# Optimization experiments

Measured on AMD Instinct MI355X. Metric: run time of the kernel, lower is better.

The kernel has to match this reference:

```python
import jax, jax.numpy as jnp
import numpy as np

WS = 8      # window size
SS = 4      # shift size
NH = 4      # num heads
EPS = 1e-5
MLP_RATIO = 4


def _win_part(x, ws):
    # x: [B,D,H,W,C] -> [B*nD*nH*nW, ws^3, C]
    B, D, H, W, C = x.shape
    x = x.reshape(B, D // ws, ws, H // ws, ws, W // ws, ws, C)
    x = x.transpose(0, 1, 3, 5, 2, 4, 6, 7)
    return x.reshape(-1, ws * ws * ws, C)


def _win_rev(w, ws, B, D, H, W):
    C = w.shape[-1]
    x = w.reshape(B, D // ws, H // ws, W // ws, ws, ws, ws, C)
    x = x.transpose(0, 1, 4, 2, 5, 3, 6, 7)
    return x.reshape(B, D, H, W, C)


def _ln(x, g, b):
    m = jnp.mean(x, axis=-1, keepdims=True)
    v = jnp.mean((x - m) ** 2, axis=-1, keepdims=True)
    return (x - m) / jnp.sqrt(v + EPS) * g + b


def _rel_index(ws):
    coords = np.stack(np.meshgrid(np.arange(ws), np.arange(ws), np.arange(ws), indexing='ij'))  # [3,ws,ws,ws]
    cf = coords.reshape(3, -1)                      # [3, ws^3]
    rel = (cf[:, :, None] - cf[:, None, :]).transpose(1, 2, 0) + (ws - 1)  # [N,N,3]
    return rel[..., 0] * (2 * ws - 1) ** 2 + rel[..., 1] * (2 * ws - 1) + rel[..., 2]


def _attn_mask(D, H, W, ws, ss):
    img = np.zeros((1, D, H, W, 1), dtype=np.float32)
    cnt = 0
    sl = (slice(0, -ws), slice(-ws, -ss), slice(-ss, None))
    for d in sl:
        for h in sl:
            for w in sl:
                img[:, d, h, w, :] = cnt
                cnt += 1
    mw = np.asarray(_win_part(jnp.asarray(img), ws))[..., 0]  # [nW, ws^3]
    diff = mw[:, None, :] - mw[:, :, None]
    return np.where(diff != 0, -100.0, 0.0).astype(np.float32)


def setup_inputs() -> dict:
    key = jax.random.key(0)
    ks = jax.random.split(key, 12)
    B, D, H, W, C = 1, 16, 64, 64, 128
    mh = MLP_RATIO * C
    s = 0.02
    return {
        'x': jax.random.normal(ks[0], (B, D, H, W, C), jnp.float32),
        'attn_mask': jnp.asarray(_attn_mask(D, H, W, WS, SS)),
        'rel_index': jnp.asarray(_rel_index(WS), jnp.int32),
        'rel_bias': jax.random.normal(ks[1], ((2 * WS - 1) ** 3, NH), jnp.float32) * s,
        'qkv_w': jax.random.normal(ks[2], (3 * C, C), jnp.float32) * s,
        'qkv_b': jnp.zeros((3 * C,), jnp.float32),
        'proj_w': jax.random.normal(ks[3], (C, C), jnp.float32) * s,
        'proj_b': jnp.zeros((C,), jnp.float32),
        'norm1_g': jnp.ones((C,), jnp.float32),
        'norm1_b': jnp.zeros((C,), jnp.float32),
        'norm2_g': jnp.ones((C,), jnp.float32),
        'norm2_b': jnp.zeros((C,), jnp.float32),
        'mlp_w1': jax.random.normal(ks[4], (mh, C), jnp.float32) * s,
        'mlp_b1': jnp.zeros((mh,), jnp.float32),
        'mlp_w2': jax.random.normal(ks[5], (C, mh), jnp.float32) * s,
        'mlp_b2': jnp.zeros((C,), jnp.float32),
    }


def reference(x, attn_mask, rel_index, rel_bias, qkv_w, qkv_b, proj_w, proj_b,
              norm1_g, norm1_b, norm2_g, norm2_b, mlp_w1, mlp_b1, mlp_w2, mlp_b2):
    B, D, H, W, C = x.shape
    ws, ss, nh = WS, SS, NH
    hd = C // nh
    scale = hd ** -0.5
    N = ws ** 3
    shortcut = x
    h = _ln(x, norm1_g, norm1_b)
    h = jnp.roll(h, (-ss, -ss, -ss), axis=(1, 2, 3))
    xw = _win_part(h, ws)                 # [B_, N, C]
    B_ = xw.shape[0]
    nW = attn_mask.shape[0]
    qkv = xw @ qkv_w.T + qkv_b            # [B_, N, 3C]
    qkv = qkv.reshape(B_, N, 3, nh, hd).transpose(2, 0, 3, 1, 4)  # [3,B_,h,N,hd]
    q, k, v = qkv[0] * scale, qkv[1], qkv[2]
    attn = jnp.einsum('bhnd,bhmd->bhnm', q, k)
    rpe = rel_bias[rel_index.reshape(-1)].reshape(N, N, nh).transpose(2, 0, 1)  # [h,N,N]
    attn = attn + rpe[None]
    attn = attn.reshape(B_ // nW, nW, nh, N, N) + attn_mask[None, :, None]
    attn = jax.nn.softmax(attn.reshape(B_, nh, N, N), axis=-1)
    out = jnp.einsum('bhnm,bhmd->bhnd', attn, v).transpose(0, 2, 1, 3).reshape(B_, N, C)
    out = out @ proj_w.T + proj_b
    out = _win_rev(out, ws, B, D, H, W)
    out = jnp.roll(out, (ss, ss, ss), axis=(1, 2, 3))
    x = shortcut + out
    h2 = _ln(x, norm2_g, norm2_b)
    h2 = jax.nn.gelu(h2 @ mlp_w1.T + mlp_b1, approximate=False)
    return x + h2 @ mlp_w2.T + mlp_b2
```

## Files before the change

kernel.cpp:

```cpp
#include <hip/hip_runtime.h>
#include <math.h>

typedef __bf16 bf16;
typedef __bf16 bf16x4 __attribute__((ext_vector_type(4)));
typedef __bf16 bf16x8 __attribute__((ext_vector_type(8)));
typedef float f32x4 __attribute__((ext_vector_type(4)));
typedef unsigned short u16;
typedef u16 u16x2 __attribute__((ext_vector_type(2)));

__device__ __forceinline__ float b2f(u16 b) {
  return (float)__builtin_bit_cast(bf16, b);
}

__global__ void sniff_k(const unsigned* __restrict__ xw_, int* __restrict__ flag) {
  int lane = threadIdx.x;
  int c = 0;
#pragma unroll
  for (int j = 0; j < 4; j++) {
    unsigned e = (xw_[lane * 4 + j] >> 7) & 0xFFu;
    c += (e >= 100u && e <= 140u) ? 1 : 0;
  }
#pragma unroll
  for (int d = 1; d < 64; d <<= 1) c += __shfl_xor(c, d);
  if (lane == 0) *flag = (c >= 150) ? 1 : 0;
}

__global__ __launch_bounds__(256) void canon_big_k(const void* __restrict__ src,
                                                   bf16* __restrict__ dst,
                                                   const int* __restrict__ flag) {
  int i = (blockIdx.x * 256 + threadIdx.x) * 8;
  if (*flag) {
    *(bf16x8*)&dst[i] = *(const bf16x8*)((const bf16*)src + i);
  } else {
    const float* s = (const float*)src + i;
    bf16x8 v;
#pragma unroll
    for (int j = 0; j < 8; j++) v[j] = (bf16)s[j];
    *(bf16x8*)&dst[i] = v;
  }
}

struct CanonArgs {
  const void* src[13];
  bf16* dst[13];
  int n[13];
};

__global__ __launch_bounds__(256) void canon_small_k(CanonArgs a,
                                                     const int* __restrict__ flag) {
  int ti = blockIdx.y;
  int i = blockIdx.x * 256 + threadIdx.x;
  if (i >= a.n[ti]) return;
  if (*flag)
    a.dst[ti][i] = ((const bf16*)a.src[ti])[i];
  else
    a.dst[ti][i] = (bf16)((const float*)a.src[ti])[i];
}

__global__ __launch_bounds__(256) void rpe_k(const int* __restrict__ ridx,
                                             const bf16* __restrict__ rbias,
                                             bf16* __restrict__ rpe) {
  int t = blockIdx.x * 256 + threadIdx.x;
  int m = t & 511, q = (t >> 9) & 511, h = t >> 18;
  rpe[t] = rbias[ridx[q * 512 + m] * 4 + h];
}

template <int ROLL>
__global__ __launch_bounds__(256) void ln_k(const bf16* __restrict__ x,
                                            const bf16* __restrict__ g,
                                            const bf16* __restrict__ bsh,
                                            bf16* __restrict__ out) {
  int wave = threadIdx.x >> 6, lane = threadIdx.x & 63;
  int tok = blockIdx.x * 4 + wave;
  size_t src;
  if (ROLL) {
    int win = tok >> 9, pos = tok & 511;
    int rd = (win >> 6) * 8 + (pos >> 6);
    int rh = ((win >> 3) & 7) * 8 + ((pos >> 3) & 7);
    int rw = (win & 7) * 8 + (pos & 7);
    int od = (rd + 4) & 15, oh = (rh + 4) & 63, ow = (rw + 4) & 63;
    src = (size_t)((od * 64 + oh) * 64 + ow) * 128;
  } else {
    src = (size_t)tok * 128;
  }
  int ch = lane * 2;
  u16x2 xv = *(const u16x2*)(x + src + ch);
  float f0 = b2f(xv[0]), f1 = b2f(xv[1]);
  float s = f0 + f1, sq = f0 * f0 + f1 * f1;
#pragma unroll
  for (int d = 1; d < 64; d <<= 1) {
    s += __shfl_xor(s, d);
    sq += __shfl_xor(sq, d);
  }
  float mean = s * (1.f / 128.f);
  float var = sq * (1.f / 128.f) - mean * mean;
  float rstd = rsqrtf(fmaxf(var, 0.f) + 1e-5f);
  u16x2 gv = *(const u16x2*)(g + ch), bv = *(const u16x2*)(bsh + ch);
  u16x2 ov;
  ov[0] = __builtin_bit_cast(u16, (bf16)((f0 - mean) * rstd * b2f(gv[0]) + b2f(bv[0])));
  ov[1] = __builtin_bit_cast(u16, (bf16)((f1 - mean) * rstd * b2f(gv[1]) + b2f(bv[1])));
  *(u16x2*)(out + (size_t)tok * 128 + ch) = ov;
}

template <int EPI, int N_, int K_>
__global__ __launch_bounds__(256) void gemm_k(const bf16* __restrict__ A,
                                              const bf16* __restrict__ B,
                                              const bf16* __restrict__ bias,
                                              void* __restrict__ outv,
                                              const bf16* __restrict__ resid,
                                              const int* __restrict__ flag) {
  __shared__ __align__(16) u16 As[128 * 72];
  __shared__ __align__(16) u16 Bs[128 * 72];
  const int t = threadIdx.x;
  const int wave = t >> 6, lane = t & 63, l15 = lane & 15, quad = lane >> 4;
  const int m0 = blockIdx.x * 128, n0 = blockIdx.y * 128;
  int fl = 0;
  if constexpr (EPI == 3) fl = *flag;
  f32x4 acc[4][4] = {};
  const int wr = (wave >> 1) * 64, wc = (wave & 1) * 64;
  const int srow = t >> 3, scol = (t & 7) * 8;
  for (int kc = 0; kc < K_; kc += 64) {
    bf16x8 av[4], bv[4];
#pragma unroll
    for (int p = 0; p < 4; p++) {
      int row = p * 32 + srow;
      av[p] = *(const bf16x8*)(A + (size_t)(m0 + row) * K_ + kc + scol);
      bv[p] = *(const bf16x8*)(B + (size_t)(n0 + row) * K_ + kc + scol);
    }
    __syncthreads();
#pragma unroll
    for (int p = 0; p < 4; p++) {
      int row = p * 32 + srow;
      *(bf16x8*)&As[row * 72 + scol] = av[p];
      *(bf16x8*)&Bs[row * 72 + scol] = bv[p];
    }
    __syncthreads();
#pragma unroll
    for (int ks = 0; ks < 2; ks++) {
      bf16x8 a[4], b[4];
#pragma unroll
      for (int i = 0; i < 4; i++) {
        a[i] = *(const bf16x8*)&As[(wr + i * 16 + l15) * 72 + ks * 32 + quad * 8];
        b[i] = *(const bf16x8*)&Bs[(wc + i * 16 + l15) * 72 + ks * 32 + quad * 8];
      }
#pragma unroll
      for (int i = 0; i < 4; i++)
#pragma unroll
        for (int j = 0; j < 4; j++)
          acc[i][j] =
              __builtin_amdgcn_mfma_f32_16x16x32_bf16(a[i], b[j], acc[i][j], 0, 0, 0);
    }
  }
  const float qscale = 0.17677669529663687f;
#pragma unroll
  for (int i = 0; i < 4; i++) {
#pragma unroll
    for (int r = 0; r < 4; r++) {
      int tok = m0 + wr + i * 16 + quad * 4 + r;
      size_t obase = 0;
      if constexpr (EPI == 1) {
        int win = tok >> 9, pos = tok & 511;
        int rd = (win >> 6) * 8 + (pos >> 6);
        int rh = ((win >> 3) & 7) * 8 + ((pos >> 3) & 7);
        int rw = (win & 7) * 8 + (pos & 7);
        int od = (rd + 4) & 15, oh = (rh + 4) & 63, ow = (rw + 4) & 63;
        obase = (size_t)((od * 64 + oh) * 64 + ow) * 128;
      } else if constexpr (EPI != 0) {
        obase = (size_t)tok * N_;
      }
#pragma unroll
      for (int j = 0; j < 4; j++) {
        int gn = n0 + wc + j * 16 + l15;
        float v = acc[i][j][r] + (float)bias[gn];
        if constexpr (EPI == 0) {
          int tensor = gn >> 7, c = gn & 127, head = c >> 5, d = c & 31;
          if (tensor == 0) v *= qscale;
          int win = tok >> 9, pos = tok & 511;
          size_t off = ((((size_t)tensor * 4 + head) * 128 + win) * 512 + pos) * 32 + d;
          ((bf16*)outv)[off] = (bf16)v;
        } else if constexpr (EPI == 1) {
          v += (float)resid[obase + gn];
          ((bf16*)outv)[obase + gn] = (bf16)v;
        } else if constexpr (EPI == 2) {
          v = 0.5f * v * (1.f + erff(v * 0.70710678118654752f));
          ((bf16*)outv)[obase + gn] = (bf16)v;
        } else {
          v += (float)resid[obase + gn];
          if (fl)
            ((bf16*)outv)[obase + gn] = (bf16)v;
          else
            ((float*)outv)[obase + gn] = v;
        }
      }
    }
  }
}

__global__ __launch_bounds__(256) void attn_k(const bf16* __restrict__ qkv,
                                              const bf16* __restrict__ rpe,
                                              bf16* __restrict__ att) {
  __shared__ __align__(16) bf16 sVt[32 * 520];
  __shared__ __align__(16) bf16 sP[4][32 * 72];
  __shared__ __align__(4) unsigned char lbl[512];
  const int t = threadIdx.x;
  const int p = blockIdx.x;
  const int win = ((p >> 7) << 3) | (p & 7);
  const int j = (p >> 3) & 15;
  const int head = j >> 2, qc = j & 3;
  const int wave = t >> 6, lane = t & 63, l15 = lane & 15, quad = lane >> 4;

  const int wd = win >> 6, wh = (win >> 3) & 7, ww = win & 7;
  const bool wm = (wd == 1) || (wh == 7) || (ww == 7);
  if (wm) {
    for (int pp = t; pp < 512; pp += 256) {
      int gd = wd * 8 + (pp >> 6), gh = wh * 8 + ((pp >> 3) & 7),
          gw = ww * 8 + (pp & 7);
      int ld = gd < 8 ? 0 : (gd < 12 ? 1 : 2);
      int lh = gh < 56 ? 0 : (gh < 60 ? 1 : 2);
      int lw = gw < 56 ? 0 : (gw < 60 ? 1 : 2);
      lbl[pp] = (unsigned char)((ld << 4) | (lh << 2) | lw);
    }
  }

  const size_t hw32 = (size_t)512 * 32;
  const bf16* qp = qkv + ((size_t)(0 * 4 + head) * 128 + win) * hw32;
  const bf16* kp = qkv + ((size_t)(1 * 4 + head) * 128 + win) * hw32;
  const bf16* vp = qkv + ((size_t)(2 * 4 + head) * 128 + win) * hw32;
  const bf16* rpeh = rpe + (size_t)head * 512 * 512;
  const int qbase = qc * 128 + wave * 32;

  {
    int kpi = t >> 3;
    int dblk = (t & 7) * 4;
    unsigned* s32 = (unsigned*)sVt;
#pragma unroll
    for (int kb = 0; kb < 8; kb++) {
      const bf16* v0 = vp + (size_t)(kb * 64 + 2 * kpi) * 32 + dblk;
      bf16x4 a = *(const bf16x4*)v0;
      bf16x4 b = *(const bf16x4*)(v0 + 32);
      int keyw = (kb * 64 + 2 * kpi) >> 1;
#pragma unroll
      for (int dd = 0; dd < 4; dd++) {
        unsigned wv = (unsigned)__builtin_bit_cast(u16, a[dd]) |
                      ((unsigned)__builtin_bit_cast(u16, b[dd]) << 16);
        s32[(dblk + dd) * 260 + keyw] = wv;
      }
    }
  }

  bf16x8 qa[2];
#pragma unroll
  for (int nt = 0; nt < 2; nt++)
    qa[nt] = *(const bf16x8*)(qp + (size_t)(qbase + nt * 16 + l15) * 32 + quad * 8);

  __syncthreads();

  int lq[2] = {0, 0};
  if (wm) {
#pragma unroll
    for (int nt = 0; nt < 2; nt++) lq[nt] = lbl[qbase + nt * 16 + l15];
  }

  f32x4 O[2][2] = {};
  float ms[2], ls[2];
#pragma unroll
  for (int nt = 0; nt < 2; nt++) {
    ms[nt] = -1e30f;
    ls[nt] = 0.f;
  }
  bf16* pw = sP[wave];

  for (int kt = 0; kt < 8; kt++) {
    f32x4 S[4][2];
#pragma unroll
    for (int mt = 0; mt < 4; mt++) {
      bf16x8 kb =
          *(const bf16x8*)(kp + (size_t)(kt * 64 + mt * 16 + l15) * 32 + quad * 8);
      int kcb = kt * 64 + mt * 16 + quad * 4;
      unsigned kl4 = 0;
      if (wm) kl4 = *(const unsigned*)&lbl[kcb];
#pragma unroll
      for (int nt = 0; nt < 2; nt++) {
        bf16x4 rv = *(const bf16x4*)(rpeh + (size_t)(qbase + nt * 16 + l15) * 512 + kcb);
        f32x4 c;
#pragma unroll
        for (int r = 0; r < 4; r++) {
          float bv = (float)rv[r];
          if (wm && (int)((kl4 >> (8 * r)) & 0xFF) != lq[nt]) bv -= 100.f;
          c[r] = bv;
        }
        S[mt][nt] = __builtin_amdgcn_mfma_f32_16x16x32_bf16(kb, qa[nt], c, 0, 0, 0);
      }
    }
#pragma unroll
    for (int nt = 0; nt < 2; nt++) {
      float mx = -1e30f;
#pragma unroll
      for (int mt = 0; mt < 4; mt++)
#pragma unroll
        for (int r = 0; r < 4; r++) mx = fmaxf(mx, S[mt][nt][r]);
      mx = fmaxf(mx, __shfl_xor(mx, 16));
      mx = fmaxf(mx, __shfl_xor(mx, 32));
      float mnew = fmaxf(ms[nt], mx);
      float alpha = __expf(ms[nt] - mnew);
      ms[nt] = mnew;
      float rs = 0.f;
#pragma unroll
      for (int mt = 0; mt < 4; mt++)
#pragma unroll
        for (int r = 0; r < 4; r++) {
          float pe = __expf(S[mt][nt][r] - mnew);
          S[mt][nt][r] = pe;
          rs += pe;
        }
      rs += __shfl_xor(rs, 16);
      rs += __shfl_xor(rs, 32);
      ls[nt] = ls[nt] * alpha + rs;
      O[0][nt] *= alpha;
      O[1][nt] *= alpha;
    }
#pragma unroll
    for (int nt = 0; nt < 2; nt++)
#pragma unroll
      for (int mt = 0; mt < 4; mt++) {
        bf16x4 pv;
#pragma unroll
        for (int r = 0; r < 4; r++) pv[r] = (bf16)S[mt][nt][r];
        *(bf16x4*)&pw[(nt * 16 + l15) * 72 + mt * 16 + quad * 4] = pv;
      }
#pragma unroll
    for (int s = 0; s < 2; s++) {
      bf16x8 va0 = *(const bf16x8*)&sVt[l15 * 520 + kt * 64 + s * 32 + quad * 8];
      bf16x8 va1 =
          *(const bf16x8*)&sVt[(16 + l15) * 520 + kt * 64 + s * 32 + quad * 8];
      bf16x8 pb0 = *(const bf16x8*)&pw[l15 * 72 + s * 32 + quad * 8];
      bf16x8 pb1 = *(const bf16x8*)&pw[(16 + l15) * 72 + s * 32 + quad * 8];
      O[0][0] = __builtin_amdgcn_mfma_f32_16x16x32_bf16(va0, pb0, O[0][0], 0, 0, 0);
      O[0][1] = __builtin_amdgcn_mfma_f32_16x16x32_bf16(va0, pb1, O[0][1], 0, 0, 0);
      O[1][0] = __builtin_amdgcn_mfma_f32_16x16x32_bf16(va1, pb0, O[1][0], 0, 0, 0);
      O[1][1] = __builtin_amdgcn_mfma_f32_16x16x32_bf16(va1, pb1, O[1][1], 0, 0, 0);
    }
  }
#pragma unroll
  for (int nt = 0; nt < 2; nt++) {
    float inv = __builtin_amdgcn_rcpf(ls[nt]);
    int q = qbase + nt * 16 + l15;
#pragma unroll
    for (int dm = 0; dm < 2; dm++) {
      bf16x4 o;
#pragma unroll
      for (int r = 0; r < 4; r++) o[r] = (bf16)(O[dm][nt][r] * inv);
      *(bf16x4*)(att + ((size_t)win * 512 + q) * 128 + head * 32 + dm * 16 +
                 quad * 4) = o;
    }
  }
}

extern "C" void kernel_launch(void* const* d_in, const int* in_sizes, int n_in,
                              void* d_out, int out_size, void* d_ws,
                              size_t ws_size, hipStream_t stream) {
  const int* rel_index = (const int*)d_in[2];
  char* w = (char*)d_ws;

  int* flag = (int*)w;
  bf16* rb_c = (bf16*)(w + (64ull << 10));
  bf16* qw_c = (bf16*)(w + (128ull << 10));
  bf16* pw_c = (bf16*)(w + (256ull << 10));
  bf16* w1_c = (bf16*)(w + (320ull << 10));
  bf16* w2_c = (bf16*)(w + (512ull << 10));
  bf16* qb_c = (bf16*)(w + (704ull << 10));
  bf16* pb_c = (bf16*)(w + (708ull << 10));
  bf16* g1_c = (bf16*)(w + (712ull << 10));
  bf16* b1n_c = (bf16*)(w + (716ull << 10));
  bf16* g2_c = (bf16*)(w + (720ull << 10));
  bf16* b2n_c = (bf16*)(w + (724ull << 10));
  bf16* mb1_c = (bf16*)(w + (728ull << 10));
  bf16* mb2_c = (bf16*)(w + (732ull << 10));
  bf16* x_c = (bf16*)(w + (1ull << 20));
  bf16* xw = (bf16*)(w + (17ull << 20));
  bf16* qkvb = (bf16*)(w + (33ull << 20));
  bf16* rpe = (bf16*)(w + (97ull << 20));
  bf16* x2 = (bf16*)(w + (99ull << 20));
  bf16* att = xw;
  bf16* h2 = xw;
  bf16* a1 = qkvb;

  sniff_k<<<1, 64, 0, stream>>>((const unsigned*)d_in[0], flag);
  canon_big_k<<<4096, 256, 0, stream>>>(d_in[0], x_c, flag);

  CanonArgs ca;
  const int srcidx[13] = {3, 4, 5, 6, 7, 8, 9, 10, 11, 12, 13, 14, 15};
  bf16* dsts[13] = {rb_c, qw_c, qb_c, pw_c, pb_c, g1_c, b1n_c,
                    g2_c, b2n_c, w1_c, mb1_c, w2_c, mb2_c};
  for (int i = 0; i < 13; i++) {
    ca.src[i] = d_in[srcidx[i]];
    ca.dst[i] = dsts[i];
    ca.n[i] = in_sizes[srcidx[i]];
  }
  canon_small_k<<<dim3(256, 13), 256, 0, stream>>>(ca, flag);

  rpe_k<<<4096, 256, 0, stream>>>(rel_index, rb_c, rpe);
  ln_k<1><<<16384, 256, 0, stream>>>(x_c, g1_c, b1n_c, xw);
  gemm_k<0, 384, 128><<<dim3(512, 3), 256, 0, stream>>>(xw, qw_c, qb_c, qkvb,
                                                        nullptr, flag);
  attn_k<<<2048, 256, 0, stream>>>(qkvb, rpe, att);
  gemm_k<1, 128, 128><<<dim3(512, 1), 256, 0, stream>>>(att, pw_c, pb_c, x2,
                                                        x_c, flag);
  ln_k<0><<<16384, 256, 0, stream>>>(x2, g2_c, b2n_c, h2);
  gemm_k<2, 512, 128><<<dim3(512, 4), 256, 0, stream>>>(h2, w1_c, mb1_c, a1,
                                                        nullptr, flag);
  gemm_k<3, 128, 512><<<dim3(512, 1), 256, 0, stream>>>(a1, w2_c, mb2_c, d_out,
                                                        x2, flag);
}
```

Baseline: 433.0 us.

## Use exp2 softmax, tanh-style GELU, A-prefetch in GEMM, halve attention V smem

Several changes at once. The attention softmax now uses exp2 by pre-scaling the RPE table, the q scale and the mask constant by log2(e). The exact erf GELU is replaced by a sigmoid-based polynomial approximation built on exp2 and rcp. The GEMM double-buffers A-tile register loads one chunk ahead. The attention kernel stages V into shared memory in two halves to shrink LDS use, which may raise occupancy but adds one extra barrier. The GELU approximation changes numerics slightly.

```diff
diff --git a/kernel.cpp b/kernel.cpp
--- a/kernel.cpp
+++ b/kernel.cpp
@@ -7,6 +7,8 @@
 typedef float f32x4 __attribute__((ext_vector_type(4)));
 typedef unsigned short u16;
 typedef u16 u16x2 __attribute__((ext_vector_type(2)));
+
+#define LOG2E 1.4426950408889634f
 
 __device__ __forceinline__ float b2f(u16 b) {
   return (float)__builtin_bit_cast(bf16, b);
@@ -62,7 +64,7 @@
                                              bf16* __restrict__ rpe) {
   int t = blockIdx.x * 256 + threadIdx.x;
   int m = t & 511, q = (t >> 9) & 511, h = t >> 18;
-  rpe[t] = rbias[ridx[q * 512 + m] * 4 + h];
+  rpe[t] = (bf16)((float)rbias[ridx[q * 512 + m] * 4 + h] * LOG2E);
 }
 
 template <int ROLL>
@@ -119,13 +121,29 @@
   f32x4 acc[4][4] = {};
   const int wr = (wave >> 1) * 64, wc = (wave & 1) * 64;
   const int srow = t >> 3, scol = (t & 7) * 8;
-  for (int kc = 0; kc < K_; kc += 64) {
-    bf16x8 av[4], bv[4];
+  constexpr int NC = K_ / 64;
+  bf16x8 avA[4], avB[4];
+#pragma unroll
+  for (int p = 0; p < 4; p++) {
+    int row = p * 32 + srow;
+    avA[p] = *(const bf16x8*)(A + (size_t)(m0 + row) * K_ + scol);
+  }
+#pragma unroll
+  for (int c = 0; c < NC; c++) {
+    const bf16x8* av = (c & 1) ? avB : avA;
+    bf16x8* avN = (c & 1) ? avA : avB;
+    if (c + 1 < NC) {
+#pragma unroll
+      for (int p = 0; p < 4; p++) {
+        int row = p * 32 + srow;
+        avN[p] = *(const bf16x8*)(A + (size_t)(m0 + row) * K_ + (c + 1) * 64 + scol);
+      }
+    }
+    bf16x8 bv[4];
 #pragma unroll
     for (int p = 0; p < 4; p++) {
       int row = p * 32 + srow;
-      av[p] = *(const bf16x8*)(A + (size_t)(m0 + row) * K_ + kc + scol);
-      bv[p] = *(const bf16x8*)(B + (size_t)(n0 + row) * K_ + kc + scol);
+      bv[p] = *(const bf16x8*)(B + (size_t)(n0 + row) * K_ + c * 64 + scol);
     }
     __syncthreads();
 #pragma unroll
@@ -151,7 +169,7 @@
               __builtin_amdgcn_mfma_f32_16x16x32_bf16(a[i], b[j], acc[i][j], 0, 0, 0);
     }
   }
-  const float qscale = 0.17677669529663687f;
+  const float qscale = 0.17677669529663687f * LOG2E;
 #pragma unroll
   for (int i = 0; i < 4; i++) {
 #pragma unroll
@@ -182,7 +200,11 @@
           v += (float)resid[obase + gn];
           ((bf16*)outv)[obase + gn] = (bf16)v;
         } else if constexpr (EPI == 2) {
-          v = 0.5f * v * (1.f + erff(v * 0.70710678118654752f));
+          float v2 = v * v;
+          float u2 = v * (2.30220806f + 0.10294323f * v2);
+          float e2 = exp2f(u2);
+          float rcp = __builtin_amdgcn_rcpf(e2 + 1.f);
+          v = v - v * rcp;
           ((bf16*)outv)[obase + gn] = (bf16)v;
         } else {
           v += (float)resid[obase + gn];
@@ -199,7 +221,7 @@
 __global__ __launch_bounds__(256) void attn_k(const bf16* __restrict__ qkv,
                                               const bf16* __restrict__ rpe,
                                               bf16* __restrict__ att) {
-  __shared__ __align__(16) bf16 sVt[32 * 520];
+  __shared__ __align__(16) bf16 sVt[32 * 264];
   __shared__ __align__(16) bf16 sP[4][32 * 72];
   __shared__ __align__(4) unsigned char lbl[512];
   const int t = threadIdx.x;
@@ -229,116 +251,115 @@
   const bf16* rpeh = rpe + (size_t)head * 512 * 512;
   const int qbase = qc * 128 + wave * 32;
 
-  {
-    int kpi = t >> 3;
-    int dblk = (t & 7) * 4;
-    unsigned* s32 = (unsigned*)sVt;
-#pragma unroll
-    for (int kb = 0; kb < 8; kb++) {
-      const bf16* v0 = vp + (size_t)(kb * 64 + 2 * kpi) * 32 + dblk;
-      bf16x4 a = *(const bf16x4*)v0;
-      bf16x4 b = *(const bf16x4*)(v0 + 32);
-      int keyw = (kb * 64 + 2 * kpi) >> 1;
-#pragma unroll
-      for (int dd = 0; dd < 4; dd++) {
-        unsigned wv = (unsigned)__builtin_bit_cast(u16, a[dd]) |
-                      ((unsigned)__builtin_bit_cast(u16, b[dd]) << 16);
-        s32[(dblk + dd) * 260 + keyw] = wv;
-      }
-    }
-  }
-
   bf16x8 qa[2];
 #pragma unroll
   for (int nt = 0; nt < 2; nt++)
     qa[nt] = *(const bf16x8*)(qp + (size_t)(qbase + nt * 16 + l15) * 32 + quad * 8);
 
-  __syncthreads();
-
+  f32x4 O[2][2] = {};
+  float ms[2] = {-1e30f, -1e30f}, ls[2] = {0.f, 0.f};
   int lq[2] = {0, 0};
-  if (wm) {
-#pragma unroll
-    for (int nt = 0; nt < 2; nt++) lq[nt] = lbl[qbase + nt * 16 + l15];
-  }
-
-  f32x4 O[2][2] = {};
-  float ms[2], ls[2];
-#pragma unroll
-  for (int nt = 0; nt < 2; nt++) {
-    ms[nt] = -1e30f;
-    ls[nt] = 0.f;
-  }
   bf16* pw = sP[wave];
 
-  for (int kt = 0; kt < 8; kt++) {
-    f32x4 S[4][2];
-#pragma unroll
-    for (int mt = 0; mt < 4; mt++) {
-      bf16x8 kb =
-          *(const bf16x8*)(kp + (size_t)(kt * 64 + mt * 16 + l15) * 32 + quad * 8);
-      int kcb = kt * 64 + mt * 16 + quad * 4;
-      unsigned kl4 = 0;
-      if (wm) kl4 = *(const unsigned*)&lbl[kcb];
+  for (int half = 0; half < 2; half++) {
+    if (half) __syncthreads();
+    {
+      int kpi = t >> 3, dblk = (t & 7) * 4;
+      unsigned* s32 = (unsigned*)sVt;
+#pragma unroll
+      for (int kb = 0; kb < 4; kb++) {
+        const bf16* v0 = vp + (size_t)(half * 256 + kb * 64 + 2 * kpi) * 32 + dblk;
+        bf16x4 a = *(const bf16x4*)v0;
+        bf16x4 b = *(const bf16x4*)(v0 + 32);
+        int keyw = kb * 32 + kpi;
+#pragma unroll
+        for (int dd = 0; dd < 4; dd++) {
+          unsigned wv = (unsigned)__builtin_bit_cast(u16, a[dd]) |
+                        ((unsigned)__builtin_bit_cast(u16, b[dd]) << 16);
+          s32[(dblk + dd) * 132 + keyw] = wv;
+        }
+      }
+    }
+    __syncthreads();
+    if (half == 0 && wm) {
+#pragma unroll
+      for (int nt = 0; nt < 2; nt++) lq[nt] = lbl[qbase + nt * 16 + l15];
+    }
+
+#pragma unroll 2
+    for (int kt4 = 0; kt4 < 4; kt4++) {
+      const int kt = half * 4 + kt4;
+      f32x4 S[4][2];
+#pragma unroll
+      for (int mt = 0; mt < 4; mt++) {
+        bf16x8 kb =
+            *(const bf16x8*)(kp + (size_t)(kt * 64 + mt * 16 + l15) * 32 + quad * 8);
+        int kcb = kt * 64 + mt * 16 + quad * 4;
+        unsigned kl4 = 0;
+        if (wm) kl4 = *(const unsigned*)&lbl[kcb];
+#pragma unroll
+        for (int nt = 0; nt < 2; nt++) {
+          bf16x4 rv =
+              *(const bf16x4*)(rpeh + (size_t)(qbase + nt * 16 + l15) * 512 + kcb);
+          f32x4 c;
+#pragma unroll
+          for (int r = 0; r < 4; r++) {
+            float bv = (float)rv[r];
+            if (wm && (int)((kl4 >> (8 * r)) & 0xFF) != lq[nt]) bv -= 144.269504f;
+            c[r] = bv;
+          }
+          S[mt][nt] = __builtin_amdgcn_mfma_f32_16x16x32_bf16(kb, qa[nt], c, 0, 0, 0);
+        }
+      }
 #pragma unroll
       for (int nt = 0; nt < 2; nt++) {
-        bf16x4 rv = *(const bf16x4*)(rpeh + (size_t)(qbase + nt * 16 + l15) * 512 + kcb);
-        f32x4 c;
-#pragma unroll
-        for (int r = 0; r < 4; r++) {
-          float bv = (float)rv[r];
-          if (wm && (int)((kl4 >> (8 * r)) & 0xFF) != lq[nt]) bv -= 100.f;
-          c[r] = bv;
+        float mx = -1e30f;
+#pragma unroll
+        for (int mt = 0; mt < 4; mt++)
+#pragma unroll
+          for (int r = 0; r < 4; r++) mx = fmaxf(mx, S[mt][nt][r]);
+        mx = fmaxf(mx, __shfl_xor(mx, 16));
+        mx = fmaxf(mx, __shfl_xor(mx, 32));
+        float mnew = fmaxf(ms[nt], mx);
+        float alpha = exp2f(ms[nt] - mnew);
+        ms[nt] = mnew;
+        float rs = 0.f;
+#pragma unroll
+        for (int mt = 0; mt < 4; mt++)
+#pragma unroll
+          for (int r = 0; r < 4; r++) {
+            float pe = exp2f(S[mt][nt][r] - mnew);
+            S[mt][nt][r] = pe;
+            rs += pe;
+          }
+        rs += __shfl_xor(rs, 16);
+        rs += __shfl_xor(rs, 32);
+        ls[nt] = ls[nt] * alpha + rs;
+        O[0][nt] *= alpha;
+        O[1][nt] *= alpha;
+      }
+#pragma unroll
+      for (int nt = 0; nt < 2; nt++)
+#pragma unroll
+        for (int mt = 0; mt < 4; mt++) {
+          bf16x4 pv;
+#pragma unroll
+          for (int r = 0; r < 4; r++) pv[r] = (bf16)S[mt][nt][r];
+          *(bf16x4*)&pw[(nt * 16 + l15) * 72 + mt * 16 + quad * 4] = pv;
         }
-        S[mt][nt] = __builtin_amdgcn_mfma_f32_16x16x32_bf16(kb, qa[nt], c, 0, 0, 0);
-      }
-    }
-#pragma unroll
-    for (int nt = 0; nt < 2; nt++) {
-      float mx = -1e30f;
-#pragma unroll
-      for (int mt = 0; mt < 4; mt++)
-#pragma unroll
-        for (int r = 0; r < 4; r++) mx = fmaxf(mx, S[mt][nt][r]);
-      mx = fmaxf(mx, __shfl_xor(mx, 16));
-      mx = fmaxf(mx, __shfl_xor(mx, 32));
-      float mnew = fmaxf(ms[nt], mx);
-      float alpha = __expf(ms[nt] - mnew);
-      ms[nt] = mnew;
-      float rs = 0.f;
-#pragma unroll
-      for (int mt = 0; mt < 4; mt++)
-#pragma unroll
-        for (int r = 0; r < 4; r++) {
-          float pe = __expf(S[mt][nt][r] - mnew);
-          S[mt][nt][r] = pe;
-          rs += pe;
-        }
-      rs += __shfl_xor(rs, 16);
-      rs += __shfl_xor(rs, 32);
-      ls[nt] = ls[nt] * alpha + rs;
-      O[0][nt] *= alpha;
-      O[1][nt] *= alpha;
-    }
-#pragma unroll
-    for (int nt = 0; nt < 2; nt++)
-#pragma unroll
-      for (int mt = 0; mt < 4; mt++) {
-        bf16x4 pv;
-#pragma unroll
-        for (int r = 0; r < 4; r++) pv[r] = (bf16)S[mt][nt][r];
-        *(bf16x4*)&pw[(nt * 16 + l15) * 72 + mt * 16 + quad * 4] = pv;
-      }
-#pragma unroll
-    for (int s = 0; s < 2; s++) {
-      bf16x8 va0 = *(const bf16x8*)&sVt[l15 * 520 + kt * 64 + s * 32 + quad * 8];
-      bf16x8 va1 =
-          *(const bf16x8*)&sVt[(16 + l15) * 520 + kt * 64 + s * 32 + quad * 8];
-      bf16x8 pb0 = *(const bf16x8*)&pw[l15 * 72 + s * 32 + quad * 8];
-      bf16x8 pb1 = *(const bf16x8*)&pw[(16 + l15) * 72 + s * 32 + quad * 8];
-      O[0][0] = __builtin_amdgcn_mfma_f32_16x16x32_bf16(va0, pb0, O[0][0], 0, 0, 0);
-      O[0][1] = __builtin_amdgcn_mfma_f32_16x16x32_bf16(va0, pb1, O[0][1], 0, 0, 0);
-      O[1][0] = __builtin_amdgcn_mfma_f32_16x16x32_bf16(va1, pb0, O[1][0], 0, 0, 0);
-      O[1][1] = __builtin_amdgcn_mfma_f32_16x16x32_bf16(va1, pb1, O[1][1], 0, 0, 0);
+#pragma unroll
+      for (int s = 0; s < 2; s++) {
+        bf16x8 va0 =
+            *(const bf16x8*)&sVt[l15 * 264 + kt4 * 64 + s * 32 + quad * 8];
+        bf16x8 va1 =
+            *(const bf16x8*)&sVt[(16 + l15) * 264 + kt4 * 64 + s * 32 + quad * 8];
+        bf16x8 pb0 = *(const bf16x8*)&pw[l15 * 72 + s * 32 + quad * 8];
+        bf16x8 pb1 = *(const bf16x8*)&pw[(16 + l15) * 72 + s * 32 + quad * 8];
+        O[0][0] = __builtin_amdgcn_mfma_f32_16x16x32_bf16(va0, pb0, O[0][0], 0, 0, 0);
+        O[0][1] = __builtin_amdgcn_mfma_f32_16x16x32_bf16(va0, pb1, O[0][1], 0, 0, 0);
+        O[1][0] = __builtin_amdgcn_mfma_f32_16x16x32_bf16(va1, pb0, O[1][0], 0, 0, 0);
+        O[1][1] = __builtin_amdgcn_mfma_f32_16x16x32_bf16(va1, pb1, O[1][1], 0, 0, 0);
+      }
     }
   }
 #pragma unroll
```

New measurement: 449.5 us. 3.8% more time.
